# Kernel tuning notes

Hardware: AMD Instinct MI355X
Metric: run time of the kernel (lower is better)

The kernel has to match this reference:

```python
import jax, jax.numpy as jnp
import numpy as np

E, D_IN, D_H, D_OUT = 8, 1024, 4096, 1024
N_TOK = 4096


def setup_inputs() -> dict:
    key = jax.random.key(0)
    ks = jax.random.split(key, 7)
    s1 = 1.0 / np.sqrt(D_IN)
    s2 = 1.0 / np.sqrt(D_H)
    return {
        "x": jax.random.normal(ks[0], (N_TOK, D_IN), dtype=jnp.float32),
        "W1": jax.random.uniform(ks[1], (E, D_IN, D_H), jnp.float32, -s1, s1),
        "b1": jax.random.uniform(ks[2], (E, D_H), jnp.float32, -s1, s1),
        "W2": jax.random.uniform(ks[3], (E, D_H, D_OUT), jnp.float32, -s2, s2),
        "b2": jax.random.uniform(ks[4], (E, D_OUT), jnp.float32, -s2, s2),
        "Wg": jax.random.uniform(ks[5], (D_IN, E), jnp.float32, -s1, s1),
        "bg": jax.random.uniform(ks[6], (E,), jnp.float32, -s1, s1),
    }


def reference(x, W1, b1, W2, b2, Wg, bg):
    # gate: [N, E] softmax over experts
    gate = jax.nn.softmax(x @ Wg + bg, axis=-1)
    # all-experts 2-layer MLP, batched over experts
    h = jax.nn.relu(jnp.einsum('ni,eih->neh', x, W1) + b1)          # [N, E, H]
    y = jnp.einsum('neh,eho->neo', h, W2) + b2                      # [N, E, O]
    # gate-weighted sum over experts
    return jnp.einsum('ne,neo->no', gate, y)                        # [N, O]
```

## Files before the change

kernel.cpp:

```cpp
#include <hip/hip_runtime.h>

#define E_EXP 8
#define D_IN 1024
#define D_H 4096
#define D_OUT 1024
#define N_TOK 4096

using f32x4  = __attribute__((ext_vector_type(4))) float;
using bf16x8 = __attribute__((ext_vector_type(8))) __bf16;
using us8    = __attribute__((ext_vector_type(8))) unsigned short;

typedef __attribute__((address_space(1))) void gvoid_t;
typedef __attribute__((address_space(3))) void lvoid_t;

__device__ __forceinline__ void async_load16(const void* g, void* l) {
    __builtin_amdgcn_global_load_lds((gvoid_t*)g, (lvoid_t*)l, 16, 0, 0);
}

__device__ __forceinline__ unsigned short f2bf(float f) {
    unsigned int x = __float_as_uint(f);
    x += 0x7fffu + ((x >> 16) & 1u);
    return (unsigned short)(x >> 16);
}

__global__ __launch_bounds__(256) void cast_x_kernel(const float* __restrict__ in,
                                                     unsigned short* __restrict__ outp) {
    int i = blockIdx.x * 256 + threadIdx.x;
    float4 f0 = ((const float4*)in)[i * 2];
    float4 f1 = ((const float4*)in)[i * 2 + 1];
    us8 u;
    u[0] = f2bf(f0.x); u[1] = f2bf(f0.y); u[2] = f2bf(f0.z); u[3] = f2bf(f0.w);
    u[4] = f2bf(f1.x); u[5] = f2bf(f1.y); u[6] = f2bf(f1.z); u[7] = f2bf(f1.w);
    ((us8*)outp)[i] = u;
}

__global__ __launch_bounds__(256) void gate_kernel(const float* __restrict__ x,
                                                   const float* __restrict__ Wg,
                                                   const float* __restrict__ bg,
                                                   float* __restrict__ gate) {
    int wave = threadIdx.x >> 6, lane = threadIdx.x & 63;
    int n = blockIdx.x * 4 + wave;
    int e = lane & 7, part = lane >> 3;
    const float* xr = x + (size_t)n * D_IN + part * (D_IN / 8);
    const float* wr = Wg + (size_t)part * (D_IN / 8) * E_EXP + e;
    float s = 0.f;
#pragma unroll 4
    for (int d = 0; d < D_IN / 8; d++) s += xr[d] * wr[d * E_EXP];
    s += __shfl_xor(s, 8);
    s += __shfl_xor(s, 16);
    s += __shfl_xor(s, 32);
    s += bg[e];
    float m = s;
    m = fmaxf(m, __shfl_xor(m, 1));
    m = fmaxf(m, __shfl_xor(m, 2));
    m = fmaxf(m, __shfl_xor(m, 4));
    float ex = __expf(s - m);
    float sum = ex;
    sum += __shfl_xor(sum, 1);
    sum += __shfl_xor(sum, 2);
    sum += __shfl_xor(sum, 4);
    if (lane < 8) gate[n * 8 + lane] = ex / sum;
}

__global__ __launch_bounds__(256) void transpose_cast64(const float* __restrict__ in,
                                                        unsigned short* __restrict__ outp,
                                                        int R, int C) {
    in   += (size_t)blockIdx.z * R * C;
    outp += (size_t)blockIdx.z * R * C;
    __shared__ float tile[64][65];
    const int t = threadIdx.x;
    const int r0 = blockIdx.y * 64, c0 = blockIdx.x * 64;
    {
        int r = t >> 4, cc = (t & 15) * 4;
#pragma unroll
        for (int p = 0; p < 4; p++) {
            float4 v = *(const float4*)(in + (size_t)(r0 + p * 16 + r) * C + c0 + cc);
            tile[p * 16 + r][cc]     = v.x;
            tile[p * 16 + r][cc + 1] = v.y;
            tile[p * 16 + r][cc + 2] = v.z;
            tile[p * 16 + r][cc + 3] = v.w;
        }
    }
    __syncthreads();
    {
        int c = t >> 3, w = t & 7;
#pragma unroll
        for (int p = 0; p < 2; p++) {
            int cc = p * 32 + c;
            us8 v;
#pragma unroll
            for (int i = 0; i < 8; i++) v[i] = f2bf(tile[w * 8 + i][cc]);
            *(us8*)(outp + (size_t)(c0 + cc) * R + r0 + w * 8) = v;
        }
    }
}

__global__ __launch_bounds__(256) void out_init_kernel(const float* __restrict__ gate,
                                                       const float* __restrict__ b2,
                                                       float* __restrict__ out) {
    int i = blockIdx.x * 256 + threadIdx.x;
    int n = i / (D_OUT / 4), o4 = i % (D_OUT / 4);
    const float* g = gate + n * 8;
    float4 s = make_float4(0.f, 0.f, 0.f, 0.f);
#pragma unroll
    for (int e = 0; e < E_EXP; e++) {
        float4 b = ((const float4*)(b2 + (size_t)e * D_OUT))[o4];
        float ge = g[e];
        s.x += ge * b.x; s.y += ge * b.y; s.z += ge * b.z; s.w += ge * b.w;
    }
    ((float4*)out)[i] = s;
}

template <int MODE>
__global__ __launch_bounds__(256, 2) void gemm_kernel(const unsigned short* __restrict__ Abase,
                                                      const unsigned short* __restrict__ Wbase,
                                                      const float* __restrict__ b1a,
                                                      const float* __restrict__ gate,
                                                      unsigned short* __restrict__ Hout,
                                                      float* __restrict__ out,
                                                      int e0, size_t hstride) {
    __shared__ __align__(16) unsigned short As[256 * 64];
    __shared__ __align__(16) unsigned short Bs[128 * 64];
    const int t = threadIdx.x;
    const int wave = t >> 6;
    const int lane = t & 63;
    const int quad = lane >> 4;
    const int l16 = lane & 15;

    const int lin = blockIdx.x;
    const int xcd = lin & 7;
    const int s = lin >> 3;
    int n_t, er, m_t;
    if (MODE == 0) {
        n_t = s & 31;
        int em = s >> 5;
        er = em >> 1;
        m_t = (em & 1) + xcd * 2;
    } else {
        n_t = s & 7;
        int em = s >> 3;
        er = em >> 1;
        m_t = (em & 1) + xcd * 2;
    }
    const int e = e0 + er;
    const int n0 = n_t * 128;
    const int m0 = m_t * 256;
    const int ld = (MODE == 0) ? D_IN : D_H;
    const int K  = (MODE == 0) ? D_IN : D_H;

    const unsigned short* A = Abase + (MODE == 1 ? (size_t)er * hstride : (size_t)0);
    const unsigned short* B = Wbase + (size_t)e * 4194304;

    const int r0 = t >> 3;
    const int gk = ((t & 7) ^ (r0 & 7)) << 3;
    const unsigned short* aP = A + (size_t)(m0 + r0) * ld + gk;
    const unsigned short* bP = B + (size_t)(n0 + r0) * ld + gk;

    const int wm = (wave & 1) * 128;
    const int wn = (wave >> 1) * 64;
    f32x4 acc[8][4] = {};

    for (int k = 0; k < K; k += 64) {
#pragma unroll
        for (int j = 0; j < 8; j++)
            async_load16(aP + k + (size_t)j * 32 * ld, &As[(j * 256 + wave * 64) * 8]);
#pragma unroll
        for (int j = 0; j < 4; j++)
            async_load16(bP + k + (size_t)j * 32 * ld, &Bs[(j * 256 + wave * 64) * 8]);
        __syncthreads();
#pragma unroll
        for (int half = 0; half < 2; half++) {
            bf16x8 af[8], bfr[4];
#pragma unroll
            for (int i = 0; i < 8; i++) {
                int row = wm + i * 16 + l16;
                af[i] = *reinterpret_cast<const bf16x8*>(
                    &As[row * 64 + (((half << 2) + quad) ^ (row & 7)) * 8]);
            }
#pragma unroll
            for (int j = 0; j < 4; j++) {
                int row = wn + j * 16 + l16;
                bfr[j] = *reinterpret_cast<const bf16x8*>(
                    &Bs[row * 64 + (((half << 2) + quad) ^ (row & 7)) * 8]);
            }
#pragma unroll
            for (int i = 0; i < 8; i++)
#pragma unroll
                for (int j = 0; j < 4; j++)
                    acc[i][j] = __builtin_amdgcn_mfma_f32_16x16x32_bf16(af[i], bfr[j], acc[i][j], 0, 0, 0);
        }
        __syncthreads();
    }

    const int mrow = m0 + wm + quad * 4;
    const int ncol = n0 + wn + l16;
    if (MODE == 0) {
        const float* bias = b1a + (size_t)e * D_H;
        unsigned short* Hbase = Hout + (size_t)er * hstride;
#pragma unroll
        for (int i = 0; i < 8; i++) {
#pragma unroll
            for (int r = 0; r < 4; r++) {
                int row = mrow + i * 16 + r;
                float g = gate[row * 8 + e];
                unsigned short* hr = Hbase + (size_t)row * D_H;
#pragma unroll
                for (int j = 0; j < 4; j++) {
                    int col = ncol + j * 16;
                    float v = fmaxf(acc[i][j][r] + bias[col], 0.f) * g;
                    hr[col] = f2bf(v);
                }
            }
        }
    } else {
#pragma unroll
        for (int i = 0; i < 8; i++) {
#pragma unroll
            for (int r = 0; r < 4; r++) {
                int row = mrow + i * 16 + r;
                float* orow = out + (size_t)row * D_OUT;
#pragma unroll
                for (int j = 0; j < 4; j++) {
                    int col = ncol + j * 16;
                    unsafeAtomicAdd(&orow[col], acc[i][j][r]);
                }
            }
        }
    }
}

extern "C" void kernel_launch(void* const* d_in, const int* in_sizes, int n_in,
                              void* d_out, int out_size, void* d_ws, size_t ws_size,
                              hipStream_t stream) {
    const float* x  = (const float*)d_in[0];
    const float* W1 = (const float*)d_in[1];
    const float* b1 = (const float*)d_in[2];
    const float* W2 = (const float*)d_in[3];
    const float* b2 = (const float*)d_in[4];
    const float* Wg = (const float*)d_in[5];
    const float* bg = (const float*)d_in[6];
    float* out = (float*)d_out;

    char* p = (char*)d_ws;
    unsigned short* xb  = (unsigned short*)p; p += (size_t)N_TOK * D_IN * 2;
    unsigned short* W1T = (unsigned short*)p; p += (size_t)E_EXP * D_IN * D_H * 2;
    unsigned short* W2T = (unsigned short*)p; p += (size_t)E_EXP * D_H * D_OUT * 2;
    float* gate         = (float*)p;          p += (size_t)N_TOK * E_EXP * 4;
    unsigned short* h   = (unsigned short*)p;

    const size_t hstride = (size_t)N_TOK * D_H;

    cast_x_kernel<<<dim3(N_TOK * D_IN / 2048), 256, 0, stream>>>(x, xb);
    gate_kernel<<<dim3(N_TOK / 4), 256, 0, stream>>>(x, Wg, bg, gate);
    transpose_cast64<<<dim3(D_H / 64, D_IN / 64, E_EXP), 256, 0, stream>>>(W1, W1T, D_IN, D_H);
    transpose_cast64<<<dim3(D_OUT / 64, D_H / 64, E_EXP), 256, 0, stream>>>(W2, W2T, D_H, D_OUT);
    out_init_kernel<<<dim3(N_TOK * D_OUT / 1024), 256, 0, stream>>>(gate, b2, out);

    for (int g = 0; g < 2; g++) {
        gemm_kernel<0><<<dim3(2048), 256, 0, stream>>>(
            xb, W1T, b1, gate, h, nullptr, g * 4, hstride);
        gemm_kernel<1><<<dim3(512), 256, 0, stream>>>(
            h, W2T, nullptr, nullptr, nullptr, out, g * 4, hstride);
    }
}
```

Baseline: 935.0 us.

## Double-buffer LDS tiles with K=32 steps to overlap async loads with MFMA

The GEMM main loop changes from a single-buffered K=64 tile to a double-buffered K=32 tile. The next tile's global-to-LDS async loads are issued before computing on the current buffer, and one barrier per iteration replaces two. The aim is to hide global load latency behind MFMA work. In exchange the loop has twice as many iterations with smaller tiles per sync, and there is a possible race if the async loads are not waited on (vmcnt) before the barrier.

```diff
diff --git a/kernel.cpp b/kernel.cpp
--- a/kernel.cpp
+++ b/kernel.cpp
@@ -119,8 +119,8 @@
                                                       unsigned short* __restrict__ Hout,
                                                       float* __restrict__ out,
                                                       int e0, size_t hstride) {
-    __shared__ __align__(16) unsigned short As[256 * 64];
-    __shared__ __align__(16) unsigned short Bs[128 * 64];
+    __shared__ __align__(16) unsigned short As[2][256 * 32];
+    __shared__ __align__(16) unsigned short Bs[2][128 * 32];
     const int t = threadIdx.x;
     const int wave = t >> 6;
     const int lane = t & 63;
@@ -151,45 +151,54 @@
     const unsigned short* A = Abase + (MODE == 1 ? (size_t)er * hstride : (size_t)0);
     const unsigned short* B = Wbase + (size_t)e * 4194304;
 
-    const int r0 = t >> 3;
-    const int gk = ((t & 7) ^ (r0 & 7)) << 3;
+    const int r0 = t >> 2;
+    const int gk = ((t & 3) ^ (r0 & 3)) << 3;
     const unsigned short* aP = A + (size_t)(m0 + r0) * ld + gk;
     const unsigned short* bP = B + (size_t)(n0 + r0) * ld + gk;
+    const int ldsOff = wave * 64 * 8;
 
     const int wm = (wave & 1) * 128;
     const int wn = (wave >> 1) * 64;
     f32x4 acc[8][4] = {};
 
-    for (int k = 0; k < K; k += 64) {
-#pragma unroll
-        for (int j = 0; j < 8; j++)
-            async_load16(aP + k + (size_t)j * 32 * ld, &As[(j * 256 + wave * 64) * 8]);
-#pragma unroll
-        for (int j = 0; j < 4; j++)
-            async_load16(bP + k + (size_t)j * 32 * ld, &Bs[(j * 256 + wave * 64) * 8]);
+    const int NIT = K / 32;
+#pragma unroll
+    for (int j = 0; j < 4; j++)
+        async_load16(aP + (size_t)(j * 64) * ld, &As[0][j * 2048 + ldsOff]);
+#pragma unroll
+    for (int j = 0; j < 2; j++)
+        async_load16(bP + (size_t)(j * 64) * ld, &Bs[0][j * 2048 + ldsOff]);
+
+    for (int it = 0; it < NIT; ++it) {
         __syncthreads();
-#pragma unroll
-        for (int half = 0; half < 2; half++) {
-            bf16x8 af[8], bfr[4];
-#pragma unroll
-            for (int i = 0; i < 8; i++) {
-                int row = wm + i * 16 + l16;
-                af[i] = *reinterpret_cast<const bf16x8*>(
-                    &As[row * 64 + (((half << 2) + quad) ^ (row & 7)) * 8]);
-            }
-#pragma unroll
-            for (int j = 0; j < 4; j++) {
-                int row = wn + j * 16 + l16;
-                bfr[j] = *reinterpret_cast<const bf16x8*>(
-                    &Bs[row * 64 + (((half << 2) + quad) ^ (row & 7)) * 8]);
-            }
-#pragma unroll
-            for (int i = 0; i < 8; i++)
-#pragma unroll
-                for (int j = 0; j < 4; j++)
-                    acc[i][j] = __builtin_amdgcn_mfma_f32_16x16x32_bf16(af[i], bfr[j], acc[i][j], 0, 0, 0);
-        }
-        __syncthreads();
+        if (it + 1 < NIT) {
+            const int kn = (it + 1) * 32;
+            const int pb = (it + 1) & 1;
+#pragma unroll
+            for (int j = 0; j < 4; j++)
+                async_load16(aP + kn + (size_t)(j * 64) * ld, &As[pb][j * 2048 + ldsOff]);
+#pragma unroll
+            for (int j = 0; j < 2; j++)
+                async_load16(bP + kn + (size_t)(j * 64) * ld, &Bs[pb][j * 2048 + ldsOff]);
+        }
+        const unsigned short* Ar = As[it & 1];
+        const unsigned short* Br = Bs[it & 1];
+        bf16x8 af[8], bfr[4];
+#pragma unroll
+        for (int i = 0; i < 8; i++) {
+            int row = wm + i * 16 + l16;
+            af[i] = *reinterpret_cast<const bf16x8*>(&Ar[row * 32 + ((quad ^ (row & 3)) * 8)]);
+        }
+#pragma unroll
+        for (int j = 0; j < 4; j++) {
+            int row = wn + j * 16 + l16;
+            bfr[j] = *reinterpret_cast<const bf16x8*>(&Br[row * 32 + ((quad ^ (row & 3)) * 8)]);
+        }
+#pragma unroll
+        for (int i = 0; i < 8; i++)
+#pragma unroll
+            for (int j = 0; j < 4; j++)
+                acc[i][j] = __builtin_amdgcn_mfma_f32_16x16x32_bf16(af[i], bfr[j], acc[i][j], 0, 0, 0);
     }
 
     const int mrow = m0 + wm + quad * 4;
```

New measurement: 1.113 ms. +19.1%, slower.
